# Kernel tuning notes

Measured on AMD Instinct MI355X. Metric: run time of the kernel, lower is better.

The kernel has to match this reference:

```python
import jax, jax.numpy as jnp
import numpy as np

EPS = 1e-08
SPARSITY = 0.1  # fraction of (node, hyperedge) incidences set to 1


def setup_inputs() -> dict:
    key = jax.random.key(0)
    k_x, k_w, k_h, k_W, k_b = jax.random.split(key, 5)
    B, N, E, Din, Dout = 8, 4096, 2048, 256, 256
    x = jax.random.normal(k_x, (B, N, Din), dtype=jnp.float32)
    edge_weight = jax.random.uniform(k_w, (E,), dtype=jnp.float32)
    H = (jax.random.uniform(k_h, (N, E)) < SPARSITY).astype(jnp.float32)
    # nn.Linear params
    bound = 1.0 / np.sqrt(Din)
    W = jax.random.uniform(k_W, (Dout, Din), minval=-bound, maxval=bound, dtype=jnp.float32)
    b = jax.random.uniform(k_b, (Dout,), minval=-bound, maxval=bound, dtype=jnp.float32)
    return {"x": x, "edge_weight": edge_weight, "H": H, "W": W, "b": b}


def _build_adjacency(H, edge_weight):
    # dv = H @ diag(w) @ 1 = H @ w ; de = H.sum(0)
    dv = H @ edge_weight                      # [N]
    de = H.sum(axis=0)                        # [E]
    dv_is = jnp.power(dv + EPS, -0.5)         # Dv^{-1/2} diagonal
    de_inv = jnp.power(de + EPS, -1.0)        # De^{-1} diagonal
    # A = Dv^{-1/2} H W De^{-1} H^T Dv^{-1/2}; apply diagonals as row/col scales
    Hw = H * (edge_weight * de_inv)[None, :]  # [N, E]
    A = (dv_is[:, None] * (Hw @ H.T)) * dv_is[None, :]  # [N, N]
    return A


def reference(x, edge_weight, H, W, b):
    A = _build_adjacency(H, edge_weight)
    xw = jnp.einsum('bnd,od->bno', x, W) + b  # Linear: [B, N, Dout]
    out = jnp.einsum('ij,bjd->bid', A, xw)    # hypergraph propagation
    return out
```

## Files before the change

kernel.cpp:

```cpp
#include <hip/hip_runtime.h>
#include <hip/hip_bf16.h>

typedef __hip_bfloat16 bf16;
typedef __bf16 bfx8 __attribute__((ext_vector_type(8)));
typedef float f32x4 __attribute__((ext_vector_type(4)));

#define BM 128

typedef __attribute__((address_space(3))) void lds_void_t;
typedef const __attribute__((address_space(1))) void gbl_void_t;

__global__ void prep_kernel(const float* __restrict__ H, const float* __restrict__ w,
                            bf16* __restrict__ HT,
                            float* __restrict__ de, float* __restrict__ dvr, int N, int E) {
    __shared__ bf16 tile[64][65];
    __shared__ float cred[4][64];
    __shared__ float rred[4][64];
    int eb = blockIdx.x * 64, nb = blockIdx.y * 64;
    int tid = threadIdx.x;
    int c = tid & 63, g = tid >> 6;

    float cs = 0.f;
#pragma unroll
    for (int k = 0; k < 16; k++) {
        int r = g + (k << 2);
        float v = H[(size_t)(nb + r) * E + eb + c];
        bf16 bv = __float2bfloat16(v);
        tile[r][c] = bv;
        cs += v;
    }
    cred[g][c] = cs;
    __syncthreads();
    if (g == 0) {
        float s = cred[0][c] + cred[1][c] + cred[2][c] + cred[3][c];
        atomicAdd(&de[eb + c], s);
    }
    float rs = 0.f;
#pragma unroll
    for (int k = 0; k < 16; k++) {
        int cc = g + (k << 2);
        rs += __bfloat162float(tile[c][cc]) * w[eb + cc];
    }
    rred[g][c] = rs;
    __syncthreads();
    if (g == 1) {
        float s = rred[0][c] + rred[1][c] + rred[2][c] + rred[3][c];
        atomicAdd(&dvr[nb + c], s);
    }
#pragma unroll
    for (int k = 0; k < 16; k++) {
        int r = g + (k << 2);
        HT[(size_t)(eb + r) * N + nb + c] = tile[c][r];
    }
}

__global__ void finalize_kernel(const float* __restrict__ dvr, const float* __restrict__ de,
                                const float* __restrict__ w, float* __restrict__ dv_is,
                                float* __restrict__ wsc, int N, int E) {
    int i = blockIdx.x * 256 + threadIdx.x;
    if (i < N) dv_is[i] = rsqrtf(dvr[i] + 1e-8f);
    if (i < E) wsc[i] = w[i] / (de[i] + 1e-8f);
}

__global__ __launch_bounds__(256) void gemm_bt_conv(
    const float* __restrict__ A, const float* __restrict__ B, int K,
    bf16* __restrict__ C, int ldc,
    const float* __restrict__ rvec, const float* __restrict__ cvec,
    long long bStride, long long cStride) {
    __shared__ __align__(16) bf16 As[BM * 40];
    __shared__ __align__(16) bf16 Bs[BM * 40];

    const float* Bp = B + (size_t)blockIdx.z * (size_t)bStride;
    bf16*        Cp = C + (size_t)blockIdx.z * (size_t)cStride;

    const int tid     = threadIdx.x;
    const int rowBase = blockIdx.y * BM;
    const int colBase = blockIdx.x * BM;
    const int wave = tid >> 6, lane = tid & 63;
    const int wr = (wave >> 1) * 64;
    const int wc = (wave & 1) * 64;
    const int lcol = lane & 15, quad = lane >> 4;

    f32x4 acc[4][4];
#pragma unroll
    for (int i = 0; i < 4; i++)
#pragma unroll
        for (int j = 0; j < 4; j++) acc[i][j] = (f32x4){0.f, 0.f, 0.f, 0.f};

    for (int k0 = 0; k0 < K; k0 += 32) {
#pragma unroll
        for (int c = 0; c < 2; c++) {
            int ch = tid + c * 256;
            int r = ch >> 2, kc = (ch & 3) << 3;
            size_t aoff = (size_t)(rowBase + r) * K + k0 + kc;
            size_t boff = (size_t)(colBase + r) * K + k0 + kc;
            f32x4 p0 = *(const f32x4*)&A[aoff];
            f32x4 p1 = *(const f32x4*)&A[aoff + 4];
            bfx8 va;
#pragma unroll
            for (int t = 0; t < 4; t++) { va[t] = (__bf16)p0[t]; va[4 + t] = (__bf16)p1[t]; }
            *(bfx8*)&As[r * 40 + kc] = va;
            f32x4 q0 = *(const f32x4*)&Bp[boff];
            f32x4 q1 = *(const f32x4*)&Bp[boff + 4];
            bfx8 vb;
#pragma unroll
            for (int t = 0; t < 4; t++) { vb[t] = (__bf16)q0[t]; vb[4 + t] = (__bf16)q1[t]; }
            *(bfx8*)&Bs[r * 40 + kc] = vb;
        }
        __syncthreads();

        bfx8 af[4], bfr[4];
#pragma unroll
        for (int i = 0; i < 4; i++)
            af[i] = *(const bfx8*)&As[(wr + i * 16 + lcol) * 40 + quad * 8];
#pragma unroll
        for (int j = 0; j < 4; j++)
            bfr[j] = *(const bfx8*)&Bs[(wc + j * 16 + lcol) * 40 + quad * 8];
#pragma unroll
        for (int i = 0; i < 4; i++)
#pragma unroll
            for (int j = 0; j < 4; j++)
                acc[i][j] = __builtin_amdgcn_mfma_f32_16x16x32_bf16(af[i], bfr[j], acc[i][j], 0, 0, 0);
        __syncthreads();
    }

#pragma unroll
    for (int i = 0; i < 4; i++) {
#pragma unroll
        for (int j = 0; j < 4; j++) {
#pragma unroll
            for (int r = 0; r < 4; r++) {
                int grow = rowBase + wr + i * 16 + quad * 4 + r;
                int gcol = colBase + wc + j * 16 + lcol;
                float v = (acc[i][j][r] + rvec[grow]) * cvec[gcol];
                Cp[(size_t)grow * ldc + gcol] = __float2bfloat16(v);
            }
        }
    }
}


#define STG_A(cb, h, u) do { \
    __builtin_amdgcn_global_load_lds((gbl_void_t*)(ga##h##0 + (size_t)(u) * 64), \
        (lds_void_t*)&SM[(cb) * 16384 + (h) * 8192 + dOff], 16, 0, 0); \
    __builtin_amdgcn_global_load_lds((gbl_void_t*)(ga##h##1 + (size_t)(u) * 64), \
        (lds_void_t*)&SM[(cb) * 16384 + (h) * 8192 + 4096 + dOff], 16, 0, 0); \
} while (0)

#define STG_B(cb, h, u) do { \
    __builtin_amdgcn_global_load_lds((gbl_void_t*)(gb##h##0 + (size_t)(u) * 64), \
        (lds_void_t*)&SM[32768 + (cb) * 16384 + (h) * 8192 + dOff], 16, 0, 0); \
    __builtin_amdgcn_global_load_lds((gbl_void_t*)(gb##h##1 + (size_t)(u) * 64), \
        (lds_void_t*)&SM[32768 + (cb) * 16384 + (h) * 8192 + 4096 + dOff], 16, 0, 0); \
} while (0)

#define LDA_(cb, qi, i, kk) \
    (*(const bfx8*)&SM[(cb) * 16384 + aBase + ((qi) * 64 + (i) * 16) * 64 + ra##kk])
#define LDB_(cb, j, kk) \
    (*(const bfx8*)&SM[32768 + (cb) * 16384 + bjb[j] + ra##kk])

#define PH_MFMA(I0, J0) do { \
    __builtin_amdgcn_s_setprio(1); \
    _Pragma("unroll") \
    for (int i_ = 0; i_ < 4; i_++) { \
        _Pragma("unroll") \
        for (int jj_ = 0; jj_ < 2; jj_++) { \
            acc[(I0) + i_][(J0) + jj_] = __builtin_amdgcn_mfma_f32_16x16x32_bf16( \
                af[i_][0], bf[(J0) + jj_][0], acc[(I0) + i_][(J0) + jj_], 0, 0, 0); \
            acc[(I0) + i_][(J0) + jj_] = __builtin_amdgcn_mfma_f32_16x16x32_bf16( \
                af[i_][1], bf[(J0) + jj_][1], acc[(I0) + i_][(J0) + jj_], 0, 0, 0); \
        } \
    } \
    __builtin_amdgcn_s_setprio(0); \
} while (0)

#define KTILE(cb, uA, uB) do { \
     \
    _Pragma("unroll") \
    for (int i_ = 0; i_ < 4; i_++) { af[i_][0] = LDA_(cb, 0, i_, 0); af[i_][1] = LDA_(cb, 0, i_, 1); } \
    _Pragma("unroll") \
    for (int j_ = 0; j_ < 2; j_++) { bf[j_][0] = LDB_(cb, j_, 0); bf[j_][1] = LDB_(cb, j_, 1); } \
    STG_A((cb) ^ 1, 0, uA); \
    __builtin_amdgcn_s_barrier(); \
    PH_MFMA(0, 0); \
    __builtin_amdgcn_s_barrier(); \
     \
    _Pragma("unroll") \
    for (int j_ = 0; j_ < 2; j_++) { bf[2 + j_][0] = LDB_(cb, 2 + j_, 0); bf[2 + j_][1] = LDB_(cb, 2 + j_, 1); } \
    STG_A((cb) ^ 1, 1, uA); \
    __builtin_amdgcn_s_barrier(); \
    PH_MFMA(0, 2); \
    __builtin_amdgcn_s_barrier(); \
     \
    _Pragma("unroll") \
    for (int i_ = 0; i_ < 4; i_++) { af[i_][0] = LDA_(cb, 1, i_, 0); af[i_][1] = LDA_(cb, 1, i_, 1); } \
    STG_B(cb, 0, uB); \
    __builtin_amdgcn_s_barrier(); \
    PH_MFMA(4, 2); \
    __builtin_amdgcn_s_barrier(); \
     \
    STG_B(cb, 1, uB); \
    __builtin_amdgcn_s_barrier(); \
    PH_MFMA(4, 0); \
    asm volatile("s_waitcnt vmcnt(4)" ::: "memory"); \
    __builtin_amdgcn_s_barrier(); \
} while (0)

__global__ __launch_bounds__(512, 2) void gemm8ph(
    const bf16* __restrict__ A, const bf16* __restrict__ Bt, int Kst, int kLen,
    bf16* __restrict__ S0, bf16* __restrict__ S1, bf16* __restrict__ S2, bf16* __restrict__ S3,
    int ldc) {
    __shared__ __align__(16) bf16 SM[65536];

    const int nx = gridDim.x, ny = gridDim.y;
    const int nwg = nx * ny * gridDim.z;
    const int lin = (blockIdx.z * ny + blockIdx.y) * nx + blockIdx.x;
    const int cpx = nwg >> 3;
    const int swz = (lin & 7) * cpx + (lin >> 3);
    const int bx = swz % nx;
    const int t1 = swz / nx;
    const int by = t1 % ny;
    const int bz = t1 / ny;
    bf16* Cs = (bz == 0) ? S0 : (bz == 1) ? S1 : (bz == 2) ? S2 : S3;
    const int kBase = bz * kLen;
    const int NT = kLen >> 6;

    const int tid = threadIdx.x;
    const int lane = tid & 63, wave = tid >> 6;
    const int lcol = lane & 15, quad = lane >> 4;
    const int wr = (wave >> 2) * 128, wc = (wave & 3) * 64;
    const int aBase = (wave >> 2) * 8192;
    const int xr = lcol & 7;

    const int rowBase = by * 256, colBase = bx * 256;

    const int ra0 = lcol * 64 + ((quad ^ xr) << 3);
    const int ra1 = lcol * 64 + (((4 + quad) ^ xr) << 3);
    int bjb[4];
#pragma unroll
    for (int j = 0; j < 4; j++) {
        int rg = wc + j * 16;
        bjb[j] = ((rg >> 7) * 8192) + ((rg & 127) * 64);
    }

    const int srow = tid >> 3, slot = tid & 7;
    const int r0 = srow, r1 = srow + 64;
    const int sx0 = (slot ^ (r0 & 7)) << 3;
    const int sx1 = (slot ^ (r1 & 7)) << 3;
    const bf16* ga00 = A + (size_t)(rowBase + r0) * Kst + kBase + sx0;
    const bf16* ga01 = A + (size_t)(rowBase + r1) * Kst + kBase + sx1;
    const bf16* ga10 = A + (size_t)(rowBase + 128 + r0) * Kst + kBase + sx0;
    const bf16* ga11 = A + (size_t)(rowBase + 128 + r1) * Kst + kBase + sx1;
    const bf16* gb00 = Bt + (size_t)(colBase + r0) * Kst + kBase + sx0;
    const bf16* gb01 = Bt + (size_t)(colBase + r1) * Kst + kBase + sx1;
    const bf16* gb10 = Bt + (size_t)(colBase + 128 + r0) * Kst + kBase + sx0;
    const bf16* gb11 = Bt + (size_t)(colBase + 128 + r1) * Kst + kBase + sx1;
    const int dOff = tid * 8;

    f32x4 acc[8][4];
#pragma unroll
    for (int i = 0; i < 8; i++)
#pragma unroll
        for (int j = 0; j < 4; j++) acc[i][j] = (f32x4){0.f, 0.f, 0.f, 0.f};
    bfx8 af[4][2], bf[4][2];

    STG_A(0, 0, 0); STG_A(0, 1, 0); STG_B(0, 0, 0); STG_B(0, 1, 0);
    STG_B(1, 0, 1); STG_B(1, 1, 1);
    asm volatile("s_waitcnt vmcnt(4)" ::: "memory");
    __builtin_amdgcn_s_barrier();

    const int nPairs = NT >> 1;
    for (int it = 0; it < nPairs; ++it) {
        int u1 = 2 * it + 1;
        int u2 = 2 * it + 2; if (u2 > NT - 1) u2 = NT - 1;
        int u3 = 2 * it + 3; if (u3 > NT - 1) u3 = NT - 1;
        KTILE(0, u1, u2);
        KTILE(1, u2, u3);
    }

#pragma unroll
    for (int i = 0; i < 8; i++) {
#pragma unroll
        for (int j = 0; j < 4; j++) {
#pragma unroll
            for (int r = 0; r < 4; r++) {
                int grow = rowBase + wr + i * 16 + quad * 4 + r;
                int gcol = colBase + wc + j * 16 + lcol;
                Cs[(size_t)grow * ldc + gcol] = __float2bfloat16(acc[i][j][r]);
            }
        }
    }
}

__global__ void combine4_kernel(const bf16* __restrict__ s0, const bf16* __restrict__ s1,
                                const bf16* __restrict__ s2, const bf16* __restrict__ s3,
                                const float* __restrict__ wsc, bf16* __restrict__ tt) {
    size_t i = ((size_t)blockIdx.x * 256 + threadIdx.x) * 8;
    int e = (int)(i & 2047);
    bfx8 a = *(const bfx8*)&s0[i];
    bfx8 b = *(const bfx8*)&s1[i];
    bfx8 c = *(const bfx8*)&s2[i];
    bfx8 d = *(const bfx8*)&s3[i];
    bfx8 v;
#pragma unroll
    for (int t = 0; t < 8; t++)
        v[t] = (__bf16)((((float)a[t] + (float)b[t]) + ((float)c[t] + (float)d[t])) * wsc[e + t]);
    *(bfx8*)&tt[i] = v;
}

__global__ void transpose_kernel(const bf16* __restrict__ src, bf16* __restrict__ dst,
                                 int R, int C) {
    __shared__ __bf16 t[64][68];
    int cb = blockIdx.x * 64, rb = blockIdx.y * 64;
    int tid = threadIdx.x;
    int lc = tid & 7, lr = tid >> 3;
#pragma unroll
    for (int p = 0; p < 2; p++) {
        int r = lr + p * 32;
        bfx8 v = *(const bfx8*)&src[(size_t)(rb + r) * C + cb + lc * 8];
#pragma unroll
        for (int q = 0; q < 8; q++) t[r][lc * 8 + q] = v[q];
    }
    __syncthreads();
#pragma unroll
    for (int p = 0; p < 2; p++) {
        int c = lr + p * 32;
        bfx8 v;
#pragma unroll
        for (int q = 0; q < 8; q++) v[q] = t[lc * 8 + q][c];
        *(bfx8*)&dst[(size_t)(cb + c) * R + rb + lc * 8] = v;
    }
}

__global__ void combine_out_kernel(const bf16* __restrict__ sA, const bf16* __restrict__ sB,
                                   const float* __restrict__ dv_is, float* __restrict__ out) {
    size_t t8 = ((size_t)blockIdx.x * 256 + threadIdx.x) * 8;
    int o = (int)(t8 & 255);
    int n = (int)((t8 >> 8) & 4095);
    int b = (int)(t8 >> 20);
    size_t si = (size_t)n * 2048 + b * 256 + o;
    bfx8 a = *(const bfx8*)&sA[si];
    bfx8 bb = *(const bfx8*)&sB[si];
    float d = dv_is[n];
    f32x4 v0, v1;
#pragma unroll
    for (int t = 0; t < 4; t++) {
        v0[t] = d * ((float)a[t] + (float)bb[t]);
        v1[t] = d * ((float)a[4 + t] + (float)bb[4 + t]);
    }
    *(f32x4*)&out[t8] = v0;
    *(f32x4*)&out[t8 + 4] = v1;
}

extern "C" void kernel_launch(void* const* d_in, const int* in_sizes, int n_in,
                              void* d_out, int out_size, void* d_ws, size_t ws_size,
                              hipStream_t stream) {
    const float* x    = (const float*)d_in[0];
    const float* ew   = (const float*)d_in[1];
    const float* H    = (const float*)d_in[2];
    const float* W    = (const float*)d_in[3];
    const float* bias = (const float*)d_in[4];

    const int N = 4096, E = 2048;

    char* ws = (char*)d_ws;
    float* de    = (float*)(ws);
    float* dvr   = (float*)(ws + 8192);
    float* dv_is = (float*)(ws + 24576);
    float* wsc   = (float*)(ws + 40960);
    bf16*  HT    = (bf16*)(ws + 65536);
    bf16*  xs_t  = (bf16*)(ws + 65536 + 16777216);
    bf16*  t_t   = (bf16*)(ws + 65536 + 33554432);

    bf16* s0 = (bf16*)d_out;
    bf16* s1 = s0 + 4194304;
    bf16* s2 = s0 + 2 * 4194304;
    bf16* s3 = s0 + 3 * 4194304;
    bf16* Hb = (bf16*)d_out;
    bf16* k5a = HT;
    bf16* k5b = xs_t;

    (void)hipMemsetAsync(ws, 0, 24576, stream);

    prep_kernel<<<dim3(E / 64, N / 64), 256, 0, stream>>>(H, ew, HT, de, dvr, N, E);
    finalize_kernel<<<dim3(16), 256, 0, stream>>>(dvr, de, ew, dv_is, wsc, N, E);

    gemm_bt_conv<<<dim3(4096 / BM, 256 / BM, 8), 256, 0, stream>>>(
        W, x, 256, xs_t, 4096, bias, dv_is, 1048576LL, 1048576LL);

    gemm8ph<<<dim3(8, 8, 4), 512, 0, stream>>>(xs_t, HT, 4096, 1024, s0, s1, s2, s3, 2048);

    combine4_kernel<<<dim3(2048), 256, 0, stream>>>(s0, s1, s2, s3, wsc, t_t);

    transpose_kernel<<<dim3(64, 32), 256, 0, stream>>>(HT, Hb, 2048, 4096);

    gemm8ph<<<dim3(8, 16, 2), 512, 0, stream>>>(Hb, t_t, 2048, 1024, k5a, k5b, k5a, k5a, 2048);

    combine_out_kernel<<<dim3(4096), 256, 0, stream>>>(k5a, k5b, dv_is, (float*)d_out);
}
```

Measured before the change: 216.1 us.

## Fuse finalize into consumers, write bf16 H in prep, drop transpose when workspace allows

Removes finalize_kernel and computes rsqrt(dv) and w/de inline in the GEMM epilogue and the combine kernels. prep_kernel also writes a row-major bf16 copy of H into the workspace, so the separate transpose kernel is skipped when the workspace is large enough. The small x@W^T GEMM is restructured so each block covers all 256 outputs for 64 nodes, and both A-staging loads in gemm8ph are issued in the first phase. This cuts launches and one full pass over H, at the cost of extra writes in prep and redundant divisions and rsqrts.

```diff
diff --git a/kernel.cpp b/kernel.cpp
--- a/kernel.cpp
+++ b/kernel.cpp
@@ -5,13 +5,11 @@
 typedef __bf16 bfx8 __attribute__((ext_vector_type(8)));
 typedef float f32x4 __attribute__((ext_vector_type(4)));
 
-#define BM 128
-
 typedef __attribute__((address_space(3))) void lds_void_t;
 typedef const __attribute__((address_space(1))) void gbl_void_t;
 
 __global__ void prep_kernel(const float* __restrict__ H, const float* __restrict__ w,
-                            bf16* __restrict__ HT,
+                            bf16* __restrict__ HT, bf16* __restrict__ Hb,
                             float* __restrict__ de, float* __restrict__ dvr, int N, int E) {
     __shared__ bf16 tile[64][65];
     __shared__ float cred[4][64];
@@ -27,6 +25,7 @@
         float v = H[(size_t)(nb + r) * E + eb + c];
         bf16 bv = __float2bfloat16(v);
         tile[r][c] = bv;
+        if (Hb) Hb[(size_t)(nb + r) * E + eb + c] = bv;
         cs += v;
     }
     cred[g][c] = cs;
@@ -54,32 +53,19 @@
     }
 }
 
-__global__ void finalize_kernel(const float* __restrict__ dvr, const float* __restrict__ de,
-                                const float* __restrict__ w, float* __restrict__ dv_is,
-                                float* __restrict__ wsc, int N, int E) {
-    int i = blockIdx.x * 256 + threadIdx.x;
-    if (i < N) dv_is[i] = rsqrtf(dvr[i] + 1e-8f);
-    if (i < E) wsc[i] = w[i] / (de[i] + 1e-8f);
-}
-
-__global__ __launch_bounds__(256) void gemm_bt_conv(
-    const float* __restrict__ A, const float* __restrict__ B, int K,
-    bf16* __restrict__ C, int ldc,
-    const float* __restrict__ rvec, const float* __restrict__ cvec,
-    long long bStride, long long cStride) {
-    __shared__ __align__(16) bf16 As[BM * 40];
-    __shared__ __align__(16) bf16 Bs[BM * 40];
-
-    const float* Bp = B + (size_t)blockIdx.z * (size_t)bStride;
-    bf16*        Cp = C + (size_t)blockIdx.z * (size_t)cStride;
-
-    const int tid     = threadIdx.x;
-    const int rowBase = blockIdx.y * BM;
-    const int colBase = blockIdx.x * BM;
+__global__ __launch_bounds__(256) void gemm_k3(
+    const float* __restrict__ W, const float* __restrict__ x,
+    const float* __restrict__ bias, const float* __restrict__ dvr,
+    bf16* __restrict__ xs_t) {
+    __shared__ __align__(16) bf16 As[256 * 40];
+    __shared__ __align__(16) bf16 Bs[64 * 40];
+
+    const int bx = blockIdx.x, z = blockIdx.y;
+    const int tid = threadIdx.x;
     const int wave = tid >> 6, lane = tid & 63;
-    const int wr = (wave >> 1) * 64;
-    const int wc = (wave & 1) * 64;
+    const int wr = wave * 64;
     const int lcol = lane & 15, quad = lane >> 4;
+    const float* xp = x + (size_t)z * 1048576 + (size_t)bx * 64 * 256;
 
     f32x4 acc[4][4];
 #pragma unroll
@@ -87,21 +73,22 @@
 #pragma unroll
         for (int j = 0; j < 4; j++) acc[i][j] = (f32x4){0.f, 0.f, 0.f, 0.f};
 
-    for (int k0 = 0; k0 < K; k0 += 32) {
-#pragma unroll
-        for (int c = 0; c < 2; c++) {
+    for (int k0 = 0; k0 < 256; k0 += 32) {
+#pragma unroll
+        for (int c = 0; c < 4; c++) {
             int ch = tid + c * 256;
             int r = ch >> 2, kc = (ch & 3) << 3;
-            size_t aoff = (size_t)(rowBase + r) * K + k0 + kc;
-            size_t boff = (size_t)(colBase + r) * K + k0 + kc;
-            f32x4 p0 = *(const f32x4*)&A[aoff];
-            f32x4 p1 = *(const f32x4*)&A[aoff + 4];
+            f32x4 p0 = *(const f32x4*)&W[(size_t)r * 256 + k0 + kc];
+            f32x4 p1 = *(const f32x4*)&W[(size_t)r * 256 + k0 + kc + 4];
             bfx8 va;
 #pragma unroll
             for (int t = 0; t < 4; t++) { va[t] = (__bf16)p0[t]; va[4 + t] = (__bf16)p1[t]; }
             *(bfx8*)&As[r * 40 + kc] = va;
-            f32x4 q0 = *(const f32x4*)&Bp[boff];
-            f32x4 q1 = *(const f32x4*)&Bp[boff + 4];
+        }
+        {
+            int r = tid >> 2, kc = (tid & 3) << 3;
+            f32x4 q0 = *(const f32x4*)&xp[(size_t)r * 256 + k0 + kc];
+            f32x4 q1 = *(const f32x4*)&xp[(size_t)r * 256 + k0 + kc + 4];
             bfx8 vb;
 #pragma unroll
             for (int t = 0; t < 4; t++) { vb[t] = (__bf16)q0[t]; vb[4 + t] = (__bf16)q1[t]; }
@@ -115,7 +102,7 @@
             af[i] = *(const bfx8*)&As[(wr + i * 16 + lcol) * 40 + quad * 8];
 #pragma unroll
         for (int j = 0; j < 4; j++)
-            bfr[j] = *(const bfx8*)&Bs[(wc + j * 16 + lcol) * 40 + quad * 8];
+            bfr[j] = *(const bfx8*)&Bs[(j * 16 + lcol) * 40 + quad * 8];
 #pragma unroll
         for (int i = 0; i < 4; i++)
 #pragma unroll
@@ -125,15 +112,16 @@
     }
 
 #pragma unroll
-    for (int i = 0; i < 4; i++) {
-#pragma unroll
-        for (int j = 0; j < 4; j++) {
+    for (int j = 0; j < 4; j++) {
+        int n = bx * 64 + j * 16 + lcol;
+        float dn = rsqrtf(dvr[n] + 1e-8f);
+#pragma unroll
+        for (int i = 0; i < 4; i++) {
 #pragma unroll
             for (int r = 0; r < 4; r++) {
-                int grow = rowBase + wr + i * 16 + quad * 4 + r;
-                int gcol = colBase + wc + j * 16 + lcol;
-                float v = (acc[i][j][r] + rvec[grow]) * cvec[gcol];
-                Cp[(size_t)grow * ldc + gcol] = __float2bfloat16(v);
+                int o = wr + i * 16 + quad * 4 + r;
+                float v = (acc[i][j][r] + bias[o]) * dn;
+                xs_t[(size_t)(z * 256 + o) * 4096 + n] = __float2bfloat16(v);
             }
         }
     }
@@ -181,13 +169,13 @@
     _Pragma("unroll") \
     for (int j_ = 0; j_ < 2; j_++) { bf[j_][0] = LDB_(cb, j_, 0); bf[j_][1] = LDB_(cb, j_, 1); } \
     STG_A((cb) ^ 1, 0, uA); \
+    STG_A((cb) ^ 1, 1, uA); \
     __builtin_amdgcn_s_barrier(); \
     PH_MFMA(0, 0); \
     __builtin_amdgcn_s_barrier(); \
      \
     _Pragma("unroll") \
     for (int j_ = 0; j_ < 2; j_++) { bf[2 + j_][0] = LDB_(cb, 2 + j_, 0); bf[2 + j_][1] = LDB_(cb, 2 + j_, 1); } \
-    STG_A((cb) ^ 1, 1, uA); \
     __builtin_amdgcn_s_barrier(); \
     PH_MFMA(0, 2); \
     __builtin_amdgcn_s_barrier(); \
@@ -294,7 +282,8 @@
 
 __global__ void combine4_kernel(const bf16* __restrict__ s0, const bf16* __restrict__ s1,
                                 const bf16* __restrict__ s2, const bf16* __restrict__ s3,
-                                const float* __restrict__ wsc, bf16* __restrict__ tt) {
+                                const float* __restrict__ w, const float* __restrict__ de,
+                                bf16* __restrict__ tt) {
     size_t i = ((size_t)blockIdx.x * 256 + threadIdx.x) * 8;
     int e = (int)(i & 2047);
     bfx8 a = *(const bfx8*)&s0[i];
@@ -303,8 +292,10 @@
     bfx8 d = *(const bfx8*)&s3[i];
     bfx8 v;
 #pragma unroll
-    for (int t = 0; t < 8; t++)
-        v[t] = (__bf16)((((float)a[t] + (float)b[t]) + ((float)c[t] + (float)d[t])) * wsc[e + t]);
+    for (int t = 0; t < 8; t++) {
+        float ws = w[e + t] / (de[e + t] + 1e-8f);
+        v[t] = (__bf16)((((float)a[t] + (float)b[t]) + ((float)c[t] + (float)d[t])) * ws);
+    }
     *(bfx8*)&tt[i] = v;
 }
 
@@ -333,7 +324,7 @@
 }
 
 __global__ void combine_out_kernel(const bf16* __restrict__ sA, const bf16* __restrict__ sB,
-                                   const float* __restrict__ dv_is, float* __restrict__ out) {
+                                   const float* __restrict__ dvr, float* __restrict__ out) {
     size_t t8 = ((size_t)blockIdx.x * 256 + threadIdx.x) * 8;
     int o = (int)(t8 & 255);
     int n = (int)((t8 >> 8) & 4095);
@@ -341,7 +332,7 @@
     size_t si = (size_t)n * 2048 + b * 256 + o;
     bfx8 a = *(const bfx8*)&sA[si];
     bfx8 bb = *(const bfx8*)&sB[si];
-    float d = dv_is[n];
+    float d = rsqrtf(dvr[n] + 1e-8f);
     f32x4 v0, v1;
 #pragma unroll
     for (int t = 0; t < 4; t++) {
@@ -364,37 +355,38 @@
     const int N = 4096, E = 2048;
 
     char* ws = (char*)d_ws;
-    float* de    = (float*)(ws);
-    float* dvr   = (float*)(ws + 8192);
-    float* dv_is = (float*)(ws + 24576);
-    float* wsc   = (float*)(ws + 40960);
-    bf16*  HT    = (bf16*)(ws + 65536);
-    bf16*  xs_t  = (bf16*)(ws + 65536 + 16777216);
-    bf16*  t_t   = (bf16*)(ws + 65536 + 33554432);
+    float* de   = (float*)(ws);
+    float* dvr  = (float*)(ws + 8192);
+    bf16*  HT   = (bf16*)(ws + 65536);
+    bf16*  xs_t = (bf16*)(ws + 65536 + 16777216);
+    bf16*  t_t  = (bf16*)(ws + 65536 + 33554432);
+    bf16*  wsHb = (bf16*)(ws + 65536 + 41943040);
+    const bool bigws = ws_size >= 58785792ull + 4096ull;
 
     bf16* s0 = (bf16*)d_out;
     bf16* s1 = s0 + 4194304;
     bf16* s2 = s0 + 2 * 4194304;
     bf16* s3 = s0 + 3 * 4194304;
-    bf16* Hb = (bf16*)d_out;
     bf16* k5a = HT;
     bf16* k5b = xs_t;
 
     (void)hipMemsetAsync(ws, 0, 24576, stream);
 
-    prep_kernel<<<dim3(E / 64, N / 64), 256, 0, stream>>>(H, ew, HT, de, dvr, N, E);
-    finalize_kernel<<<dim3(16), 256, 0, stream>>>(dvr, de, ew, dv_is, wsc, N, E);
-
-    gemm_bt_conv<<<dim3(4096 / BM, 256 / BM, 8), 256, 0, stream>>>(
-        W, x, 256, xs_t, 4096, bias, dv_is, 1048576LL, 1048576LL);
+    prep_kernel<<<dim3(E / 64, N / 64), 256, 0, stream>>>(
+        H, ew, HT, bigws ? wsHb : nullptr, de, dvr, N, E);
+
+    gemm_k3<<<dim3(64, 8), 256, 0, stream>>>(W, x, bias, dvr, xs_t);
 
     gemm8ph<<<dim3(8, 8, 4), 512, 0, stream>>>(xs_t, HT, 4096, 1024, s0, s1, s2, s3, 2048);
 
-    combine4_kernel<<<dim3(2048), 256, 0, stream>>>(s0, s1, s2, s3, wsc, t_t);
-
-    transpose_kernel<<<dim3(64, 32), 256, 0, stream>>>(HT, Hb, 2048, 4096);
-
-    gemm8ph<<<dim3(8, 16, 2), 512, 0, stream>>>(Hb, t_t, 2048, 1024, k5a, k5b, k5a, k5a, 2048);
-
-    combine_out_kernel<<<dim3(4096), 256, 0, stream>>>(k5a, k5b, dv_is, (float*)d_out);
-}
+    combine4_kernel<<<dim3(2048), 256, 0, stream>>>(s0, s1, s2, s3, ew, de, t_t);
+
+    bf16* HbP = bigws ? wsHb : (bf16*)d_out;
+    if (!bigws) {
+        transpose_kernel<<<dim3(64, 32), 256, 0, stream>>>(HT, HbP, 2048, 4096);
+    }
+
+    gemm8ph<<<dim3(8, 16, 2), 512, 0, stream>>>(HbP, t_t, 2048, 1024, k5a, k5b, k5a, k5a, 2048);
+
+    combine_out_kernel<<<dim3(4096), 256, 0, stream>>>(k5a, k5b, dvr, (float*)d_out);
+}
```

Result: no change. 219.9 us (+1.8%).
